# Optimization experiments

Measured on AMD Instinct MI355X. Metric: run time of the kernel, lower is better.

The kernel has to match this reference:

```python
import jax, jax.numpy as jnp
import numpy as np

MARGIN = 1.0
EPS = 1e-6


def _cos(a, b):
    # Row-wise cosine similarity, matching torch.nn.CosineSimilarity semantics:
    # dot / max(||a|| * ||b||, eps)
    num = jnp.sum(a * b, axis=-1)
    den = jnp.maximum(jnp.linalg.norm(a, axis=-1) * jnp.linalg.norm(b, axis=-1), EPS)
    return num / den


def setup_inputs() -> dict:
    key = jax.random.key(0)
    k1, k2, k3 = jax.random.split(key, 3)
    B, D = 16384, 1024
    output = jax.random.normal(k1, (B, D), dtype=jnp.float32)
    target = jax.random.normal(k2, (B, D), dtype=jnp.float32)
    # offset in [0, B-1); j = (i + 1 + neg_idx) % B guarantees j != i, uniform over the rest
    neg_idx = jax.random.randint(k3, (B,), 0, B - 1, dtype=jnp.int64)
    return {"output": output, "target": target, "neg_idx": neg_idx}


def reference(output, target, neg_idx):
    B = output.shape[0]
    j = (jnp.arange(B) + 1 + neg_idx) % B  # random negative index, j != i
    t_neg = target[j]                       # gather negative label embeddings [B, D]
    hinge = jax.nn.relu(MARGIN - _cos(target, output) + _cos(t_neg, output))
    return jnp.sum(hinge) / B
```

## Files before the change

### kernel.cpp

```cpp
#include <hip/hip_runtime.h>


#define EPS 1e-6f

typedef float f4 __attribute__((ext_vector_type(4)));

#define DPP_STEP(x, ctrl, rm, bm)                                             \
    x += __int_as_float(__builtin_amdgcn_update_dpp(                          \
        0, __float_as_int(x), (ctrl), (rm), (bm), true))

__device__ __forceinline__ float dpp_wave_sum(float x) {
    DPP_STEP(x, 0x111, 0xf, 0xf);
    DPP_STEP(x, 0x112, 0xf, 0xf);
    DPP_STEP(x, 0x114, 0xf, 0xe);
    DPP_STEP(x, 0x118, 0xf, 0xc);
    DPP_STEP(x, 0x142, 0xa, 0xf);
    DPP_STEP(x, 0x143, 0xc, 0xf);
    return x;
}

__global__ __launch_bounds__(256, 8) void hinge_cos_kernel(
    const float* __restrict__ outm,
    const float* __restrict__ tgt,
    const int*   __restrict__ negidx,
    float* __restrict__ res,
    int B, int D, float invB) {

    const int lane = threadIdx.x & 63;
    const int wave = threadIdx.x >> 6;
    const int i    = blockIdx.x * 4 + wave;

    float h = 0.f;
    if (i < B) {
        const int g = negidx[i];

        const f4* o4 = (const f4*)(outm + (size_t)i * D);
        const f4* t4 = (const f4*)(tgt  + (size_t)i * D);

        f4 o[4], t[4], n[4];
#pragma unroll
        for (int k = 0; k < 4; ++k) o[k] = o4[lane + 64 * k];
#pragma unroll
        for (int k = 0; k < 4; ++k) t[k] = t4[lane + 64 * k];

        int j = i + 1 + g; if (j >= B) j -= B;
        const f4* n4 = (const f4*)(tgt + (size_t)j * D);
#pragma unroll
        for (int k = 0; k < 4; ++k) n[k] = n4[lane + 64 * k];

        float dto = 0.f, dno = 0.f, oo = 0.f, tt = 0.f, nn = 0.f;
#pragma unroll
        for (int k = 0; k < 4; ++k) {
            dto += o[k].x*t[k].x + o[k].y*t[k].y + o[k].z*t[k].z + o[k].w*t[k].w;
            dno += o[k].x*n[k].x + o[k].y*n[k].y + o[k].z*n[k].z + o[k].w*n[k].w;
            oo  += o[k].x*o[k].x + o[k].y*o[k].y + o[k].z*o[k].z + o[k].w*o[k].w;
            tt  += t[k].x*t[k].x + t[k].y*t[k].y + t[k].z*t[k].z + t[k].w*t[k].w;
            nn  += n[k].x*n[k].x + n[k].y*n[k].y + n[k].z*n[k].z + n[k].w*n[k].w;
        }
        dto = dpp_wave_sum(dto);
        dno = dpp_wave_sum(dno);
        oo  = dpp_wave_sum(oo);
        tt  = dpp_wave_sum(tt);
        nn  = dpp_wave_sum(nn);
        float no = sqrtf(oo);
        float hv = 1.f - dto / fmaxf(sqrtf(tt) * no, EPS)
                       + dno / fmaxf(sqrtf(nn) * no, EPS);
        h = fmaxf(hv, 0.f);
    }

    __shared__ float red[4];
    if (lane == 63) red[wave] = h;
    __syncthreads();
    if (threadIdx.x == 0) {
        float s = red[0] + red[1] + red[2] + red[3];
        atomicAdd(res, s * invB);
    }
}

extern "C" void kernel_launch(void* const* d_in, const int* in_sizes, int n_in,
                              void* d_out, int out_size, void* d_ws, size_t ws_size,
                              hipStream_t stream) {
    const float* outm   = (const float*)d_in[0];
    const float* tgt    = (const float*)d_in[1];
    const int*   negidx = (const int*)d_in[2];
    float* res = (float*)d_out;

    const int B = in_sizes[2];
    const int D = in_sizes[0] / B;

    (void)hipMemsetAsync(res, 0, sizeof(float), stream);

    const int blocks = (B + 3) / 4;
    hinge_cos_kernel<<<blocks, 256, 0, stream>>>(outm, tgt, negidx, res, B, D,
                                                 1.0f / (float)B);
}
```

Before: 172.4 us.

## Process four rows per wave with double-buffered inline-asm SGPR-based loads

Each wave now handles four rows strided across the grid instead of one. It issues raw global_load_dwordx4 via inline asm with SGPR base addresses and explicit vmcnt waits, double-buffering two rows so loads overlap with the dot-product reductions. The grid shrinks by four, which also cuts the number of atomic adds. This raises register pressure (launch bounds drop to 2) and relies on hand-written waitcnt placement and a hardcoded D=1024 offset layout.

Result: faster. 148.4 us (-13.9%).

```diff
diff --git a/kernel.cpp b/kernel.cpp
--- a/kernel.cpp
+++ b/kernel.cpp
@@ -1,4 +1,5 @@
 #include <hip/hip_runtime.h>
+#include <stdint.h>
 
 
 #define EPS 1e-6f
@@ -19,57 +20,140 @@
     return x;
 }
 
-__global__ __launch_bounds__(256, 8) void hinge_cos_kernel(
+__device__ __forceinline__ uint64_t to_sgpr(const void* p) {
+    uint64_t x = (uint64_t)p;
+    uint32_t lo = __builtin_amdgcn_readfirstlane((uint32_t)x);
+    uint32_t hi = __builtin_amdgcn_readfirstlane((uint32_t)(x >> 32));
+    return ((uint64_t)hi << 32) | lo;
+}
+
+#define LOAD4S(d0, d1, d2, d3, voff, base)                                    \
+    asm volatile("global_load_dwordx4 %0, %4, %5\n\t"                         \
+                 "global_load_dwordx4 %1, %4, %5 offset:1024\n\t"             \
+                 "global_load_dwordx4 %2, %4, %5 offset:2048\n\t"             \
+                 "global_load_dwordx4 %3, %4, %5 offset:3072"                 \
+                 : "=&v"(d0), "=&v"(d1), "=&v"(d2), "=&v"(d3)                 \
+                 : "v"(voff), "s"(base))
+
+#define ISSUE_ROW(P, ob, tb, nb)                                              \
+    LOAD4S(P##o0, P##o1, P##o2, P##o3, voff, ob);                             \
+    LOAD4S(P##t0, P##t1, P##t2, P##t3, voff, tb);                             \
+    LOAD4S(P##n0, P##n1, P##n2, P##n3, voff, nb)
+
+#define ACC1(o, t, n)                                                         \
+    dto += o.x*t.x + o.y*t.y + o.z*t.z + o.w*t.w;                             \
+    dno += o.x*n.x + o.y*n.y + o.z*n.z + o.w*n.w;                             \
+    oo  += o.x*o.x + o.y*o.y + o.z*o.z + o.w*o.w;                             \
+    tt  += t.x*t.x + t.y*t.y + t.z*t.z + t.w*t.w;                             \
+    nn  += n.x*n.x + n.y*n.y + n.z*n.z + n.w*n.w
+
+#define CONSUME_ROW(P)                                                        \
+    do {                                                                      \
+        float dto = 0.f, dno = 0.f, oo = 0.f, tt = 0.f, nn = 0.f;             \
+        ACC1(P##o0, P##t0, P##n0); ACC1(P##o1, P##t1, P##n1);                 \
+        ACC1(P##o2, P##t2, P##n2); ACC1(P##o3, P##t3, P##n3);                 \
+        dto = dpp_wave_sum(dto);                                              \
+        dno = dpp_wave_sum(dno);                                              \
+        oo  = dpp_wave_sum(oo);                                               \
+        tt  = dpp_wave_sum(tt);                                               \
+        nn  = dpp_wave_sum(nn);                                               \
+        float no = sqrtf(oo);                                                 \
+        float h  = 1.f - dto / fmaxf(sqrtf(tt) * no, EPS)                     \
+                       + dno / fmaxf(sqrtf(nn) * no, EPS);                    \
+        if (lane == 63) acc += fmaxf(h, 0.f);                                 \
+    } while (0)
+
+#define WAIT(N)                                                               \
+    asm volatile("s_waitcnt vmcnt(" #N ")");                                  \
+    __builtin_amdgcn_sched_barrier(0)
+
+__global__ __launch_bounds__(256, 2) void hinge_cos_kernel(
     const float* __restrict__ outm,
     const float* __restrict__ tgt,
     const int*   __restrict__ negidx,
     float* __restrict__ res,
     int B, int D, float invB) {
 
-    const int lane = threadIdx.x & 63;
-    const int wave = threadIdx.x >> 6;
-    const int i    = blockIdx.x * 4 + wave;
+    const int lane  = threadIdx.x & 63;
+    const int wave  = threadIdx.x >> 6;
+    const int gwave = blockIdx.x * 4 + wave;
+    const int nwav  = gridDim.x * 4;
 
-    float h = 0.f;
-    if (i < B) {
-        const int g = negidx[i];
+    const int i0 = gwave;
+    const int i1 = i0 + nwav;
+    const int i2 = i1 + nwav;
+    const int i3 = i2 + nwav;
 
-        const f4* o4 = (const f4*)(outm + (size_t)i * D);
-        const f4* t4 = (const f4*)(tgt  + (size_t)i * D);
+    float acc = 0.f;
 
-        f4 o[4], t[4], n[4];
+    if (i3 < B) {
+        int g0 = negidx[i0], g1 = negidx[i1], g2 = negidx[i2], g3 = negidx[i3];
+        int j0 = i0 + 1 + g0; if (j0 >= B) j0 -= B;
+        int j1 = i1 + 1 + g1; if (j1 >= B) j1 -= B;
+        int j2 = i2 + 1 + g2; if (j2 >= B) j2 -= B;
+        int j3 = i3 + 1 + g3; if (j3 >= B) j3 -= B;
+
+        const uint64_t o0b = to_sgpr(outm + (size_t)i0 * D);
+        const uint64_t t0b = to_sgpr(tgt  + (size_t)i0 * D);
+        const uint64_t n0b = to_sgpr(tgt  + (size_t)j0 * D);
+        const uint64_t o1b = to_sgpr(outm + (size_t)i1 * D);
+        const uint64_t t1b = to_sgpr(tgt  + (size_t)i1 * D);
+        const uint64_t n1b = to_sgpr(tgt  + (size_t)j1 * D);
+        const uint64_t o2b = to_sgpr(outm + (size_t)i2 * D);
+        const uint64_t t2b = to_sgpr(tgt  + (size_t)i2 * D);
+        const uint64_t n2b = to_sgpr(tgt  + (size_t)j2 * D);
+        const uint64_t o3b = to_sgpr(outm + (size_t)i3 * D);
+        const uint64_t t3b = to_sgpr(tgt  + (size_t)i3 * D);
+        const uint64_t n3b = to_sgpr(tgt  + (size_t)j3 * D);
+
+        const int voff = lane * 16;
+
+        f4 Ao0, Ao1, Ao2, Ao3, At0, At1, At2, At3, An0, An1, An2, An3;
+        f4 Bo0, Bo1, Bo2, Bo3, Bt0, Bt1, Bt2, Bt3, Bn0, Bn1, Bn2, Bn3;
+
+        ISSUE_ROW(A, o0b, t0b, n0b);
+        ISSUE_ROW(B, o1b, t1b, n1b);
+
+        WAIT(12);
+        CONSUME_ROW(A);
+        ISSUE_ROW(A, o2b, t2b, n2b);
+
+        WAIT(12);
+        CONSUME_ROW(B);
+        ISSUE_ROW(B, o3b, t3b, n3b);
+
+        WAIT(12);
+        CONSUME_ROW(A);
+
+        WAIT(0);
+        CONSUME_ROW(B);
+    } else {
+        int idx[4] = {i0, i1, i2, i3};
+        for (int r = 0; r < 4; ++r) {
+            int i = idx[r];
+            if (i >= B) break;
+            int g = negidx[i];
+            int j = i + 1 + g; if (j >= B) j -= B;
+            const f4* o4 = (const f4*)(outm + (size_t)i * D);
+            const f4* t4 = (const f4*)(tgt  + (size_t)i * D);
+            const f4* n4 = (const f4*)(tgt  + (size_t)j * D);
+            float dto = 0.f, dno = 0.f, oo = 0.f, tt = 0.f, nn = 0.f;
 #pragma unroll
-        for (int k = 0; k < 4; ++k) o[k] = o4[lane + 64 * k];
-#pragma unroll
-        for (int k = 0; k < 4; ++k) t[k] = t4[lane + 64 * k];
-
-        int j = i + 1 + g; if (j >= B) j -= B;
-        const f4* n4 = (const f4*)(tgt + (size_t)j * D);
-#pragma unroll
-        for (int k = 0; k < 4; ++k) n[k] = n4[lane + 64 * k];
-
-        float dto = 0.f, dno = 0.f, oo = 0.f, tt = 0.f, nn = 0.f;
-#pragma unroll
-        for (int k = 0; k < 4; ++k) {
-            dto += o[k].x*t[k].x + o[k].y*t[k].y + o[k].z*t[k].z + o[k].w*t[k].w;
-            dno += o[k].x*n[k].x + o[k].y*n[k].y + o[k].z*n[k].z + o[k].w*n[k].w;
-            oo  += o[k].x*o[k].x + o[k].y*o[k].y + o[k].z*o[k].z + o[k].w*o[k].w;
-            tt  += t[k].x*t[k].x + t[k].y*t[k].y + t[k].z*t[k].z + t[k].w*t[k].w;
-            nn  += n[k].x*n[k].x + n[k].y*n[k].y + n[k].z*n[k].z + n[k].w*n[k].w;
+            for (int k = 0; k < 4; ++k) {
+                f4 o = o4[lane + 64*k], t = t4[lane + 64*k], n = n4[lane + 64*k];
+                ACC1(o, t, n);
+            }
+            dto = dpp_wave_sum(dto); dno = dpp_wave_sum(dno);
+            oo = dpp_wave_sum(oo); tt = dpp_wave_sum(tt); nn = dpp_wave_sum(nn);
+            float no = sqrtf(oo);
+            float h = 1.f - dto / fmaxf(sqrtf(tt) * no, EPS)
+                          + dno / fmaxf(sqrtf(nn) * no, EPS);
+            if (lane == 63) acc += fmaxf(h, 0.f);
         }
-        dto = dpp_wave_sum(dto);
-        dno = dpp_wave_sum(dno);
-        oo  = dpp_wave_sum(oo);
-        tt  = dpp_wave_sum(tt);
-        nn  = dpp_wave_sum(nn);
-        float no = sqrtf(oo);
-        float hv = 1.f - dto / fmaxf(sqrtf(tt) * no, EPS)
-                       + dno / fmaxf(sqrtf(nn) * no, EPS);
-        h = fmaxf(hv, 0.f);
     }
 
     __shared__ float red[4];
-    if (lane == 63) red[wave] = h;
+    if (lane == 63) red[wave] = acc;
     __syncthreads();
     if (threadIdx.x == 0) {
         float s = red[0] + red[1] + red[2] + red[3];
@@ -90,7 +174,8 @@
 
     (void)hipMemsetAsync(res, 0, sizeof(float), stream);
 
-    const int blocks = (B + 3) / 4;
+    const int nwav   = (B + 3) / 4;
+    const int blocks = (nwav + 3) / 4;
     hinge_cos_kernel<<<blocks, 256, 0, stream>>>(outm, tgt, negidx, res, B, D,
                                                  1.0f / (float)B);
 }
```
